# Optimization experiments

Measured on AMD Instinct MI355X. Metric: run time of the kernel, lower is better.

Reference implementation:

```python
import jax, jax.numpy as jnp
import numpy as np

B, S, D, H = 16, 784, 768, 12
DH = D // H  # 64


def rotate_half(x):
    # (x1, x2, x3, x4) -> (-x2, x1, -x4, x3), interleaved
    x_even = x[..., ::2]
    x_odd = x[..., 1::2]
    return jnp.stack((-x_odd, x_even), axis=-1).reshape(x.shape)


def setup_inputs() -> dict:
    key = jax.random.key(0)
    ks = jax.random.split(key, 12)
    s = 0.02
    return {
        "hidden_states": jax.random.normal(ks[0], (B, S, D), jnp.float32),
        "rotary_pos_emb": jax.random.uniform(ks[1], (B, S, DH), jnp.float32) * 6.28,
        "wq": jax.random.normal(ks[2], (D, D), jnp.float32) * s,
        "bq": jax.random.normal(ks[3], (D,), jnp.float32) * s,
        "wk": jax.random.normal(ks[4], (D, D), jnp.float32) * s,
        "bk": jax.random.normal(ks[5], (D,), jnp.float32) * s,
        "wv": jax.random.normal(ks[6], (D, D), jnp.float32) * s,
        "bv": jax.random.normal(ks[7], (D,), jnp.float32) * s,
        "wo": jax.random.normal(ks[8], (D, D), jnp.float32) * s,
        "bo": jax.random.normal(ks[9], (D,), jnp.float32) * s,
    }


def reference(hidden_states, rotary_pos_emb, wq, bq, wk, bk, wv, bv, wo, bo):
    scale = DH ** -0.5
    # Linear: x @ W^T + b; reshape to [B, H, S, DH]
    def proj(w, b):
        y = jnp.einsum("bsd,ed->bse", hidden_states, w) + b
        return y.reshape(B, S, H, DH).transpose(0, 2, 1, 3)

    q = proj(wq, bq)
    k = proj(wk, bk)
    v = proj(wv, bv)

    # RoPE: freqs [B, S, DH] -> [B, 1, S, DH] broadcast over heads
    cos = jnp.cos(rotary_pos_emb)[:, None, :, :]
    sin = jnp.sin(rotary_pos_emb)[:, None, :, :]
    q = q * cos + rotate_half(q) * sin
    k = k * cos + rotate_half(k) * sin

    attn = jnp.einsum("bhqd,bhkd->bhqk", q, k) * scale
    attn = jax.nn.softmax(attn, axis=-1)
    out = jnp.einsum("bhqk,bhkd->bhqd", attn, v)
    out = out.transpose(0, 2, 1, 3).reshape(B, S, D)
    out = jnp.einsum("bsd,ed->bse", out, wo) + bo
    return out
```

## Files before the change

### kernel.cpp

```cpp
#include <hip/hip_runtime.h>
#include <cstdint>
#include <cstddef>

constexpr int kB  = 16;
constexpr int kS  = 784;
constexpr int kD  = 768;
constexpr int kH  = 12;
constexpr int kM  = kB * kS;
constexpr int kSP = 832;

typedef __attribute__((ext_vector_type(8))) short bf16x8;
typedef __attribute__((ext_vector_type(4))) float floatx4;

__device__ __forceinline__ unsigned short f2bf(float x) {
    union { float f; unsigned int u; } v; v.f = x;
    unsigned int r = v.u + 0x7fffu + ((v.u >> 16) & 1u);
    return (unsigned short)(r >> 16);
}
__device__ __forceinline__ float bf2f(unsigned short h) {
    union { unsigned int u; float f; } v; v.u = ((unsigned int)h) << 16;
    return v.f;
}

__device__ __forceinline__ float fast_exp2(float x) {
#if __has_builtin(__builtin_amdgcn_exp2f)
    return __builtin_amdgcn_exp2f(x);
#else
    return __expf(x * 0.69314718055994531f);
#endif
}

__device__ __forceinline__ unsigned cvtpk(float lo, float hi) {
    unsigned r;
    asm("v_cvt_pk_bf16_f32 %0, %1, %2" : "=v"(r) : "v"(lo), "v"(hi));
    return r;
}
__device__ __forceinline__ void pl32(unsigned &a, unsigned &b) {
    asm("v_permlane32_swap_b32 %0, %1" : "+v"(a), "+v"(b));
}
__device__ __forceinline__ void pl16(unsigned &a, unsigned &b) {
    asm("v_permlane16_swap_b32 %0, %1" : "+v"(a), "+v"(b));
}
__device__ __forceinline__ bf16x8 mk8(unsigned a, unsigned b, unsigned c, unsigned d) {
    union { unsigned u[4]; bf16x8 v; } f;
    f.u[0] = a; f.u[1] = b; f.u[2] = c; f.u[3] = d; return f.v;
}

__device__ __forceinline__ void gload_lds16(const void* g, void* l) {
    __builtin_amdgcn_global_load_lds(
        (const __attribute__((address_space(1))) void*)g,
        (__attribute__((address_space(3))) void*)l,
        16, 0, 0);
}

constexpr int kHsF4   = (kM * kD) / 4;
constexpr int kWF4    = (kD * kD) / 4;
constexpr int kPreTot = kHsF4 + 4 * kWF4 + (kM * 64) / 4;

__global__ __launch_bounds__(256)
void convert_pre(const float* __restrict__ hs, const float* __restrict__ rot,
                 const float* __restrict__ wq, const float* __restrict__ wk,
                 const float* __restrict__ wv, const float* __restrict__ wo,
                 const float* __restrict__ bq, const float* __restrict__ bk,
                 const float* __restrict__ bv,
                 unsigned short* __restrict__ hsB, unsigned short* __restrict__ wB,
                 unsigned int* __restrict__ csT, float* __restrict__ biasC)
{
    const int i = blockIdx.x * 256 + threadIdx.x;
    if (i < kHsF4) {
        float4 v = ((const float4*)hs)[i];
        ushort4 o = { f2bf(v.x), f2bf(v.y), f2bf(v.z), f2bf(v.w) };
        ((ushort4*)hsB)[i] = o;
    } else if (i < kHsF4 + 4 * kWF4) {
        const int j = i - kHsF4;
        const int w = j / kWF4, jj = j - w * kWF4;
        const float* src = (w == 0) ? wq : (w == 1) ? wk : (w == 2) ? wv : wo;
        float4 v = ((const float4*)src)[jj];
        ushort4 o = { f2bf(v.x), f2bf(v.y), f2bf(v.z), f2bf(v.w) };
        ((ushort4*)(wB + (size_t)w * (kD * kD)))[jj] = o;
    } else if (i < kPreTot) {
        const int j = i - kHsF4 - 4 * kWF4;
        float4 v = ((const float4*)rot)[j];
        float a[4] = { v.x, v.y, v.z, v.w };
        #pragma unroll
        for (int e = 0; e < 4; ++e) {
            float s, c;
            __sincosf(a[e], &s, &c);
            csT[j * 4 + e] = (unsigned)f2bf(c) | ((unsigned)f2bf(s) << 16);
        }
    } else {
        const int j = i - kPreTot;
        if (j < 3 * kD)
            biasC[j] = (j < kD) ? bq[j] : (j < 2 * kD) ? bk[j - kD] : bv[j - 2 * kD];
    }
}

enum { MODE_QKV = 0, MODE_OUT = 1 };

#define BARR  __builtin_amdgcn_s_barrier()
#define LGK0  asm volatile("s_waitcnt lgkmcnt(0)" ::: "memory")
#define VM4   asm volatile("s_waitcnt vmcnt(4)" ::: "memory")
#define VM0   asm volatile("s_waitcnt vmcnt(0)" ::: "memory")
#define PRIO1 __builtin_amdgcn_s_setprio(1)
#define PRIO0 __builtin_amdgcn_s_setprio(0)

#define LDA4(KS, RB, MQ) do{ \
  afr[0]=*(const bf16x8*)(rdA##KS+(RB)+((MQ)+0)*4096); \
  afr[1]=*(const bf16x8*)(rdA##KS+(RB)+((MQ)+1)*4096); \
  afr[2]=*(const bf16x8*)(rdA##KS+(RB)+((MQ)+2)*4096); \
  afr[3]=*(const bf16x8*)(rdA##KS+(RB)+((MQ)+3)*4096); }while(0)

#define LDB4(KS, RB) do{ \
  bfr[0]=*(const bf16x8*)(rdB##KS+(RB)); \
  bfr[1]=*(const bf16x8*)(rdB##KS+(RB)+8192); \
  bfr[2]=*(const bf16x8*)(rdB##KS+(RB)+16384); \
  bfr[3]=*(const bf16x8*)(rdB##KS+(RB)+24576); }while(0)

#define MFMA16(MQ) do{ _Pragma("unroll") for(int nt=0;nt<4;++nt){ \
  acc[(MQ)  ][nt]=__builtin_amdgcn_mfma_f32_16x16x32_bf16(afr[0],bfr[nt],acc[(MQ)  ][nt],0,0,0); \
  acc[(MQ)+1][nt]=__builtin_amdgcn_mfma_f32_16x16x32_bf16(afr[1],bfr[nt],acc[(MQ)+1][nt],0,0,0); \
  acc[(MQ)+2][nt]=__builtin_amdgcn_mfma_f32_16x16x32_bf16(afr[2],bfr[nt],acc[(MQ)+2][nt],0,0,0); \
  acc[(MQ)+3][nt]=__builtin_amdgcn_mfma_f32_16x16x32_bf16(afr[3],bfr[nt],acc[(MQ)+3][nt],0,0,0); \
}}while(0)

#define KTILE(RB, SB, KT) do{ \
   LDA4(0, RB, 0); LDB4(0, RB); \
    if ((KT) <= 10) { stA(1, (KT)+1, SB); stB(1, (KT)+1, SB); } \
    BARR; LGK0; PRIO1; MFMA16(0); PRIO0; BARR; \
   LDA4(0, RB, 4); \
    BARR; LGK0; PRIO1; MFMA16(4); PRIO0; BARR; \
   LDA4(1, RB, 0); LDB4(1, RB); \
    BARR; LGK0; PRIO1; MFMA16(0); PRIO0; BARR; \
   LDA4(1, RB, 4); \
    if ((KT) <= 9) { stA(0, (KT)+2, RB); stB(0, (KT)+2, RB); VM4; } \
    else if ((KT) == 10) { VM0; } \
    BARR; LGK0; PRIO1; MFMA16(4); PRIO0; BARR; \
}while(0)

template<int MODE>
__global__ __launch_bounds__(512, 2)
void gemm8(const unsigned short* __restrict__ A, const unsigned short* __restrict__ W,
           const float* __restrict__ bias, const unsigned int* __restrict__ csT,
           unsigned short* __restrict__ Qp, unsigned short* __restrict__ Kp,
           unsigned short* __restrict__ Vtp, float* __restrict__ Op)
{
    constexpr int NTL = (MODE == MODE_QKV) ? 9 : 3;

    __shared__ unsigned short SM[65536];

    const int lin   = blockIdx.x;
    const int group = lin / (8 * NTL);
    const int rem   = lin - group * (8 * NTL);
    int m_tile, n_tile;
    if (group < 6) { m_tile = group * 8 + (rem & 7); n_tile = rem >> 3; }
    else           { m_tile = 48; n_tile = rem; }
    const int m0 = m_tile * 256;
    const int n0 = n_tile * 256;

    const int tid  = threadIdx.x;
    const int wave = tid >> 6;
    const int lane = tid & 63;
    const int quad = lane >> 4, l16 = lane & 15;
    const int wm = wave & 1;
    const int wn = wave >> 1;

    const int l8  = lane >> 3;
    const int sc  = (lane & 7) ^ l8;
    const unsigned short* gA0 = A + (size_t)(m0 + wave * 16 + l8) * kD + sc * 8;
    const unsigned short* gA1 = gA0 + (size_t)8 * kD;
    const unsigned short* gB0 = W + (size_t)(n0 + wave * 16 + l8) * kD + sc * 8;
    const unsigned short* gB1 = gB0 + (size_t)8 * kD;
    char* smc = (char*)SM;

    auto stA = [&](int h, int kt, int bufoff) {
        const int off = h * 98304 + kt * 64;
        gload_lds16(gA0 + off, smc + bufoff + h * 16384 + wave * 2048);
        gload_lds16(gA1 + off, smc + bufoff + h * 16384 + wave * 2048 + 1024);
    };
    auto stB = [&](int h, int kt, int bufoff) {
        const int off = h * 98304 + kt * 64;
        gload_lds16(gB0 + off, smc + 65536 + bufoff + h * 16384 + wave * 2048);
        gload_lds16(gB1 + off, smc + 65536 + bufoff + h * 16384 + wave * 2048 + 1024);
    };

    const int swz0 = ((quad    ) ^ (l16 & 7)) * 16;
    const int swz1 = ((quad + 4) ^ (l16 & 7)) * 16;
    const char* rdA0 = (const char*)SM + (wm * 16 + l16) * 128 + swz0;
    const char* rdA1 = (const char*)SM + (wm * 16 + l16) * 128 + swz1;
    const char* rdB0 = (const char*)SM + 65536 + (wn * 16 + l16) * 128 + swz0;
    const char* rdB1 = (const char*)SM + 65536 + (wn * 16 + l16) * 128 + swz1;

    floatx4 acc[8][4];
    #pragma unroll
    for (int m = 0; m < 8; ++m)
        #pragma unroll
        for (int nt = 0; nt < 4; ++nt)
            acc[m][nt] = {0.f, 0.f, 0.f, 0.f};
    bf16x8 afr[4], bfr[4];

    stA(0, 0, 0);      stB(0, 0, 0);
    stA(1, 0, 0);      stB(1, 0, 0);
    stA(0, 1, 32768);  stB(0, 1, 32768);
    VM4;
    BARR;

    #pragma unroll
    for (int ktp = 0; ktp < 6; ++ktp) {
        KTILE(0,     32768, ktp * 2);
        KTILE(32768, 0,     ktp * 2 + 1);
    }

    if constexpr (MODE == MODE_OUT) {
        #pragma unroll
        for (int nt = 0; nt < 4; ++nt) {
            const int n = n0 + nt * 64 + wn * 16 + l16;
            const float bv = bias[n];
            #pragma unroll
            for (int m = 0; m < 8; ++m)
                #pragma unroll
                for (int r = 0; r < 4; ++r) {
                    const int mm = m0 + m * 32 + wm * 16 + quad * 4 + r;
                    Op[(size_t)mm * kD + n] = acc[m][nt][r] + bv;
                }
        }
    } else {
        const int proj = n_tile / 3;
        if (proj < 2) {
            unsigned short* dst = proj ? Kp : Qp;
            const float scale = proj ? 1.0f : 0.125f * 1.44269504088896341f;
            #pragma unroll
            for (int nt = 0; nt < 4; ++nt) {
                const int n = n0 + nt * 64 + wn * 16 + l16;
                const float bv = bias[n];
                const int col = n - proj * kD;
                const int dh = col & 63;
                const int odd = l16 & 1;
                #pragma unroll
                for (int m = 0; m < 8; ++m)
                    #pragma unroll
                    for (int r = 0; r < 4; ++r) {
                        const int mm = m0 + m * 32 + wm * 16 + quad * 4 + r;
                        const float val = acc[m][nt][r] + bv;
                        const float px = __shfl_xor(val, 1);
                        const unsigned u = csT[(size_t)mm * 64 + dh];
                        const float c = bf2f((unsigned short)(u & 0xffffu));
                        const float s = bf2f((unsigned short)(u >> 16));
                        const float out = odd ? (val * c + px * s) : (val * c - px * s);
                        dst[(size_t)mm * kD + col] = f2bf(out * scale);
                    }
            }
        } else {
            #pragma unroll
            for (int nt = 0; nt < 4; ++nt) {
                const int n = n0 + nt * 64 + wn * 16 + l16;
                const float bv = bias[n];
                const int col = n - 2 * kD;
                const int h = col >> 6, dh = col & 63;
                #pragma unroll
                for (int m = 0; m < 8; ++m) {
                    const int m_r0 = m0 + m * 32 + wm * 16 + quad * 4;
                    const int b = m_r0 / kS;
                    const int s = m_r0 - b * kS;
                    ushort4 pk;
                    pk.x = f2bf(acc[m][nt][0] + bv);
                    pk.y = f2bf(acc[m][nt][1] + bv);
                    pk.z = f2bf(acc[m][nt][2] + bv);
                    pk.w = f2bf(acc[m][nt][3] + bv);
                    *(ushort4*)(Vtp + (size_t)((b * kH + h) * 64 + dh) * kSP + s) = pk;
                }
            }
        }
    }
}

__global__ __launch_bounds__(256)
void flash_attn(const unsigned short* __restrict__ Qg,
                const unsigned short* __restrict__ Kg,
                const unsigned short* __restrict__ Vtg,
                unsigned short* __restrict__ Og)
{
    __shared__ unsigned short KV[3][8192];

    const int lin   = blockIdx.x;
    const int group = lin / 56;
    const int rem   = lin - group * 56;
    const int bh = group * 8 + (rem & 7);
    const int qt = rem >> 3;
    const int b = bh / kH, h = bh - b * kH;
    const int tid = threadIdx.x, wave = tid >> 6, lane = tid & 63;
    const int quad = lane >> 4, l16 = lane & 15;
    const int q0 = qt * 128;
    const size_t rowBase = (size_t)(b * kS) * kD + h * 64;

    #pragma unroll
    for (int j = 0; j < 4; ++j) {
        const int idx = (wave * 4 + j) * 64 + lane;
        const int row = idx >> 3, slot = idx & 7, seg = slot ^ (row & 7);
        gload_lds16(Qg + rowBase + (size_t)(q0 + row) * kD + seg * 8,
                    &KV[0][(wave * 4 + j) * 512]);
    }
    __syncthreads();
    bf16x8 aq[2][2];
    #pragma unroll
    for (int mt = 0; mt < 2; ++mt)
        #pragma unroll
        for (int ch = 0; ch < 2; ++ch) {
            const int row = wave * 32 + mt * 16 + l16;
            const int slot = (ch * 4 + quad) ^ (row & 7);
            aq[mt][ch] = *(const bf16x8*)&KV[0][row * 64 + slot * 8];
        }
    __syncthreads();

    const int cidx0 = wave * 128 + lane;
    const int crow0 = cidx0 >> 3, cseg0 = (cidx0 & 7) ^ (crow0 & 7);
    const int cidx1 = cidx0 + 64;
    const int crow1 = cidx1 >> 3, cseg1 = (cidx1 & 7) ^ (crow1 & 7);

    auto stage = [&](int kt, int buf) {
        const int kr = kt * 64;
        gload_lds16(Kg + rowBase + (size_t)(kr + crow0) * kD + cseg0 * 8,
                    &KV[buf][wave * 1024]);
        gload_lds16(Vtg + (size_t)(bh * 64 + crow0) * kSP + kr + cseg0 * 8,
                    &KV[buf][4096 + wave * 1024]);
        gload_lds16(Kg + rowBase + (size_t)(kr + crow1) * kD + cseg1 * 8,
                    &KV[buf][wave * 1024 + 512]);
        gload_lds16(Vtg + (size_t)(bh * 64 + crow1) * kSP + kr + cseg1 * 8,
                    &KV[buf][4096 + wave * 1024 + 512]);
    };

    stage(0, 0);
    stage(1, 1);

    floatx4 oacc[2][4];
    #pragma unroll
    for (int mt = 0; mt < 2; ++mt)
        #pragma unroll
        for (int nt = 0; nt < 4; ++nt)
            oacc[mt][nt] = {0.f, 0.f, 0.f, 0.f};
    floatx4 lsum[2];
    lsum[0] = {0.f, 0.f, 0.f, 0.f};
    lsum[1] = {0.f, 0.f, 0.f, 0.f};
    const bf16x8 onesb = { 16256, 16256, 16256, 16256,
                           16256, 16256, 16256, 16256 };

    int cur = 0;
    int pre = 2;
    for (int kt = 0; kt < 13; ++kt) {
        asm volatile("s_barrier" ::: "memory");
        if (kt < 11) stage(kt + 2, pre);
        if (kt < 11)       asm volatile("s_waitcnt vmcnt(8)" ::: "memory");
        else if (kt == 11) asm volatile("s_waitcnt vmcnt(4)" ::: "memory");
        else               asm volatile("s_waitcnt vmcnt(0)" ::: "memory");
        asm volatile("s_barrier" ::: "memory");

        const unsigned short* Ks = &KV[cur][0];
        const unsigned short* Vs = &KV[cur][4096];

        bf16x8 bk[4][2];
        #pragma unroll
        for (int nt = 0; nt < 4; ++nt)
            #pragma unroll
            for (int ch = 0; ch < 2; ++ch) {
                const int row = nt * 16 + l16;
                const int slot = (ch * 4 + quad) ^ (row & 7);
                bk[nt][ch] = *(const bf16x8*)&Ks[row * 64 + slot * 8];
            }

        floatx4 sc[4][2];
        __builtin_amdgcn_s_setprio(1);
        #pragma unroll
        for (int nt = 0; nt < 4; ++nt)
            #pragma unroll
            for (int mt = 0; mt < 2; ++mt) {
                sc[nt][mt] = {0.f, 0.f, 0.f, 0.f};
                sc[nt][mt] = __builtin_amdgcn_mfma_f32_16x16x32_bf16(
                    bk[nt][0], aq[mt][0], sc[nt][mt], 0, 0, 0);
                sc[nt][mt] = __builtin_amdgcn_mfma_f32_16x16x32_bf16(
                    bk[nt][1], aq[mt][1], sc[nt][mt], 0, 0, 0);
            }
        __builtin_amdgcn_s_setprio(0);

        if (kt == 12) {
            #pragma unroll
            for (int nt = 1; nt < 4; ++nt)
                #pragma unroll
                for (int mt = 0; mt < 2; ++mt)
                    #pragma unroll
                    for (int r = 0; r < 4; ++r) sc[nt][mt][r] = -1e30f;
        }

        #pragma unroll
        for (int nt = 0; nt < 4; ++nt)
            #pragma unroll
            for (int mt = 0; mt < 2; ++mt)
                #pragma unroll
                for (int r = 0; r < 4; ++r)
                    sc[nt][mt][r] = fast_exp2(sc[nt][mt][r]);

        bf16x8 ap[2][2];
        #pragma unroll
        for (int mt = 0; mt < 2; ++mt) {
            unsigned L0 = cvtpk(sc[0][mt][0], sc[0][mt][1]);
            unsigned H0 = cvtpk(sc[0][mt][2], sc[0][mt][3]);
            unsigned L1 = cvtpk(sc[1][mt][0], sc[1][mt][1]);
            unsigned H1 = cvtpk(sc[1][mt][2], sc[1][mt][3]);
            unsigned L2 = cvtpk(sc[2][mt][0], sc[2][mt][1]);
            unsigned H2 = cvtpk(sc[2][mt][2], sc[2][mt][3]);
            unsigned L3 = cvtpk(sc[3][mt][0], sc[3][mt][1]);
            unsigned H3 = cvtpk(sc[3][mt][2], sc[3][mt][3]);
            pl32(L0, L1); pl16(L0, L1);
            pl32(H0, H1); pl16(H0, H1);
            ap[mt][0] = mk8(L0, H0, L1, H1);
            pl32(L2, L3); pl16(L2, L3);
            pl32(H2, H3); pl16(H2, H3);
            ap[mt][1] = mk8(L2, H2, L3, H3);
        }

        __builtin_amdgcn_s_setprio(1);
        #pragma unroll
        for (int ks = 0; ks < 2; ++ks) {
            #pragma unroll
            for (int nt = 0; nt < 4; ++nt) {
                const int row = nt * 16 + l16;
                const int slot = (ks * 4 + quad) ^ (row & 7);
                const bf16x8 bv = *(const bf16x8*)&Vs[row * 64 + slot * 8];
                #pragma unroll
                for (int mt = 0; mt < 2; ++mt)
                    oacc[mt][nt] = __builtin_amdgcn_mfma_f32_16x16x32_bf16(
                        ap[mt][ks], bv, oacc[mt][nt], 0, 0, 0);
            }
            #pragma unroll
            for (int mt = 0; mt < 2; ++mt)
                lsum[mt] = __builtin_amdgcn_mfma_f32_16x16x32_bf16(
                    ap[mt][ks], onesb, lsum[mt], 0, 0, 0);
        }
        __builtin_amdgcn_s_setprio(0);

        cur = (cur == 2) ? 0 : cur + 1;
        pre = (pre == 2) ? 0 : pre + 1;
    }

    #pragma unroll
    for (int mt = 0; mt < 2; ++mt)
        #pragma unroll
        for (int r = 0; r < 4; ++r) {
            const int srow = q0 + wave * 32 + mt * 16 + quad * 4 + r;
            if (srow < kS) {
                const float inv = 1.0f / lsum[mt][r];
                #pragma unroll
                for (int nt = 0; nt < 4; ++nt)
                    Og[rowBase + (size_t)srow * kD + nt * 16 + l16] =
                        f2bf(oacc[mt][nt][r] * inv);
            }
        }
}

extern "C" void kernel_launch(void* const* d_in, const int* in_sizes, int n_in,
                              void* d_out, int out_size, void* d_ws, size_t ws_size,
                              hipStream_t stream)
{
    (void)in_sizes; (void)n_in; (void)out_size; (void)ws_size;
    const float* hs  = (const float*)d_in[0];
    const float* rot = (const float*)d_in[1];
    const float* wq  = (const float*)d_in[2];
    const float* bq  = (const float*)d_in[3];
    const float* wk  = (const float*)d_in[4];
    const float* bk  = (const float*)d_in[5];
    const float* wv  = (const float*)d_in[6];
    const float* bv  = (const float*)d_in[7];
    const float* wo  = (const float*)d_in[8];
    const float* bo  = (const float*)d_in[9];

    char* ws = (char*)d_ws;
    unsigned short* hsB  = (unsigned short*)ws;
    unsigned short* wB   = (unsigned short*)(ws + 19267584);
    unsigned int*   csT  = (unsigned int*)(ws + 23986176);
    float*          biasC= (float*)(ws + 27197440);
    unsigned short* Q    = (unsigned short*)(ws + 27206656);
    unsigned short* K    = (unsigned short*)(ws + 46474240);
    unsigned short* Vt   = (unsigned short*)(ws + 65741824);
    unsigned short* O    = hsB;

    convert_pre<<<dim3(12505), dim3(256), 0, stream>>>(hs, rot, wq, wk, wv, wo, bq, bk, bv,
                                                       hsB, wB, csT, biasC);
    gemm8<MODE_QKV><<<dim3(441), dim3(512), 0, stream>>>(
        hsB, wB, biasC, csT, Q, K, Vt, nullptr);
    flash_attn<<<dim3(7 * 192), dim3(256), 0, stream>>>(Q, K, Vt, O);
    gemm8<MODE_OUT><<<dim3(147), dim3(512), 0, stream>>>(
        O, wB + 3 * kD * kD, bo, nullptr, nullptr, nullptr, nullptr, (float*)d_out);
}
```

Baseline: 246.2 us.

## Replace 256x256 8-wave GEMM with 128x128 4-wave triple-buffered GEMM

Both projection GEMMs drop the 256x256 tile (512 threads, 128 KB LDS, K-step 64, double buffer). They now use 128x128 tiles with 256 threads, K-step 32 and a triple-buffered LDS ring of 48 KB with a new swizzle. The launch bound asks for three blocks per CU. The goal is more blocks (1764/588 instead of 441/147) to fix the wave-quantization tail on 256 CUs and raise occupancy. The cost is lower arithmetic intensity per tile, more global and L2 traffic, and more barriers per unit of MFMA work.

Result: slower. 269.5 us (+9.5%).

```diff
diff --git a/kernel.cpp b/kernel.cpp
--- a/kernel.cpp
+++ b/kernel.cpp
@@ -104,58 +104,38 @@
 #define PRIO1 __builtin_amdgcn_s_setprio(1)
 #define PRIO0 __builtin_amdgcn_s_setprio(0)
 
-#define LDA4(KS, RB, MQ) do{ \
-  afr[0]=*(const bf16x8*)(rdA##KS+(RB)+((MQ)+0)*4096); \
-  afr[1]=*(const bf16x8*)(rdA##KS+(RB)+((MQ)+1)*4096); \
-  afr[2]=*(const bf16x8*)(rdA##KS+(RB)+((MQ)+2)*4096); \
-  afr[3]=*(const bf16x8*)(rdA##KS+(RB)+((MQ)+3)*4096); }while(0)
-
-#define LDB4(KS, RB) do{ \
-  bfr[0]=*(const bf16x8*)(rdB##KS+(RB)); \
-  bfr[1]=*(const bf16x8*)(rdB##KS+(RB)+8192); \
-  bfr[2]=*(const bf16x8*)(rdB##KS+(RB)+16384); \
-  bfr[3]=*(const bf16x8*)(rdB##KS+(RB)+24576); }while(0)
-
-#define MFMA16(MQ) do{ _Pragma("unroll") for(int nt=0;nt<4;++nt){ \
-  acc[(MQ)  ][nt]=__builtin_amdgcn_mfma_f32_16x16x32_bf16(afr[0],bfr[nt],acc[(MQ)  ][nt],0,0,0); \
-  acc[(MQ)+1][nt]=__builtin_amdgcn_mfma_f32_16x16x32_bf16(afr[1],bfr[nt],acc[(MQ)+1][nt],0,0,0); \
-  acc[(MQ)+2][nt]=__builtin_amdgcn_mfma_f32_16x16x32_bf16(afr[2],bfr[nt],acc[(MQ)+2][nt],0,0,0); \
-  acc[(MQ)+3][nt]=__builtin_amdgcn_mfma_f32_16x16x32_bf16(afr[3],bfr[nt],acc[(MQ)+3][nt],0,0,0); \
-}}while(0)
-
-#define KTILE(RB, SB, KT) do{ \
-   LDA4(0, RB, 0); LDB4(0, RB); \
-    if ((KT) <= 10) { stA(1, (KT)+1, SB); stB(1, (KT)+1, SB); } \
-    BARR; LGK0; PRIO1; MFMA16(0); PRIO0; BARR; \
-   LDA4(0, RB, 4); \
-    BARR; LGK0; PRIO1; MFMA16(4); PRIO0; BARR; \
-   LDA4(1, RB, 0); LDB4(1, RB); \
-    BARR; LGK0; PRIO1; MFMA16(0); PRIO0; BARR; \
-   LDA4(1, RB, 4); \
-    if ((KT) <= 9) { stA(0, (KT)+2, RB); stB(0, (KT)+2, RB); VM4; } \
-    else if ((KT) == 10) { VM0; } \
-    BARR; LGK0; PRIO1; MFMA16(4); PRIO0; BARR; \
+#define KTILE4(CUR, NX2, KT) do{ \
+    if ((KT) <= 21) stg((KT) + 2, NX2); \
+    _Pragma("unroll") for (int m = 0; m < 4; ++m) \
+        afr[m] = *(const bf16x8*)(rdA + (CUR)*16384 + m*1024); \
+    _Pragma("unroll") for (int nt = 0; nt < 4; ++nt) \
+        bfr[nt] = *(const bf16x8*)(rdB + (CUR)*16384 + nt*1024); \
+    BARR; LGK0; PRIO1; \
+    _Pragma("unroll") for (int m = 0; m < 4; ++m) \
+        _Pragma("unroll") for (int nt = 0; nt < 4; ++nt) \
+            acc[m][nt] = __builtin_amdgcn_mfma_f32_16x16x32_bf16( \
+                afr[m], bfr[nt], acc[m][nt], 0, 0, 0); \
+    PRIO0; \
+    if ((KT) <= 21) { VM4; } else if ((KT) == 22) { VM0; } \
+    BARR; \
 }while(0)
 
 template<int MODE>
-__global__ __launch_bounds__(512, 2)
-void gemm8(const unsigned short* __restrict__ A, const unsigned short* __restrict__ W,
+__global__ __launch_bounds__(256, 3)
+void gemm4(const unsigned short* __restrict__ A, const unsigned short* __restrict__ W,
            const float* __restrict__ bias, const unsigned int* __restrict__ csT,
            unsigned short* __restrict__ Qp, unsigned short* __restrict__ Kp,
            unsigned short* __restrict__ Vtp, float* __restrict__ Op)
 {
-    constexpr int NTL = (MODE == MODE_QKV) ? 9 : 3;
-
-    __shared__ unsigned short SM[65536];
-
-    const int lin   = blockIdx.x;
-    const int group = lin / (8 * NTL);
-    const int rem   = lin - group * (8 * NTL);
-    int m_tile, n_tile;
-    if (group < 6) { m_tile = group * 8 + (rem & 7); n_tile = rem >> 3; }
-    else           { m_tile = 48; n_tile = rem; }
-    const int m0 = m_tile * 256;
-    const int n0 = n_tile * 256;
+    constexpr int NTL = (MODE == MODE_QKV) ? 18 : 6;
+
+    __shared__ unsigned short SM[24576];
+
+    const int lin    = blockIdx.x;
+    const int m_tile = lin / NTL;
+    const int n_tile = lin - m_tile * NTL;
+    const int m0 = m_tile * 128;
+    const int n0 = n_tile * 128;
 
     const int tid  = threadIdx.x;
     const int wave = tid >> 6;
@@ -164,82 +144,77 @@
     const int wm = wave & 1;
     const int wn = wave >> 1;
 
-    const int l8  = lane >> 3;
-    const int sc  = (lane & 7) ^ l8;
-    const unsigned short* gA0 = A + (size_t)(m0 + wave * 16 + l8) * kD + sc * 8;
-    const unsigned short* gA1 = gA0 + (size_t)8 * kD;
-    const unsigned short* gB0 = W + (size_t)(n0 + wave * 16 + l8) * kD + sc * 8;
-    const unsigned short* gB1 = gB0 + (size_t)8 * kD;
+    const int srow = wave * 16 + (lane >> 2);
+    const int sc   = (lane & 3) ^ ((lane >> 3) & 3);
+    const unsigned short* gA0 = A + (size_t)(m0 + srow) * kD + sc * 8;
+    const unsigned short* gA1 = gA0 + (size_t)64 * kD;
+    const unsigned short* gB0 = W + (size_t)(n0 + srow) * kD + sc * 8;
+    const unsigned short* gB1 = gB0 + (size_t)64 * kD;
     char* smc = (char*)SM;
 
-    auto stA = [&](int h, int kt, int bufoff) {
-        const int off = h * 98304 + kt * 64;
-        gload_lds16(gA0 + off, smc + bufoff + h * 16384 + wave * 2048);
-        gload_lds16(gA1 + off, smc + bufoff + h * 16384 + wave * 2048 + 1024);
+    auto stg = [&](int kt, int buf) {
+        const int off = kt * 32;
+        char* base = smc + buf * 16384;
+        gload_lds16(gA0 + off, base + wave * 1024);
+        gload_lds16(gA1 + off, base + 4096  + wave * 1024);
+        gload_lds16(gB0 + off, base + 8192  + wave * 1024);
+        gload_lds16(gB1 + off, base + 12288 + wave * 1024);
     };
-    auto stB = [&](int h, int kt, int bufoff) {
-        const int off = h * 98304 + kt * 64;
-        gload_lds16(gB0 + off, smc + 65536 + bufoff + h * 16384 + wave * 2048);
-        gload_lds16(gB1 + off, smc + 65536 + bufoff + h * 16384 + wave * 2048 + 1024);
-    };
-
-    const int swz0 = ((quad    ) ^ (l16 & 7)) * 16;
-    const int swz1 = ((quad + 4) ^ (l16 & 7)) * 16;
-    const char* rdA0 = (const char*)SM + (wm * 16 + l16) * 128 + swz0;
-    const char* rdA1 = (const char*)SM + (wm * 16 + l16) * 128 + swz1;
-    const char* rdB0 = (const char*)SM + 65536 + (wn * 16 + l16) * 128 + swz0;
-    const char* rdB1 = (const char*)SM + 65536 + (wn * 16 + l16) * 128 + swz1;
-
-    floatx4 acc[8][4];
+
+    const int sw = (quad ^ ((l16 >> 1) & 3)) * 16;
+    const char* rdA = smc + (wm * 64 + l16) * 64 + sw;
+    const char* rdB = smc + 8192 + (wn * 64 + l16) * 64 + sw;
+
+    floatx4 acc[4][4];
     #pragma unroll
-    for (int m = 0; m < 8; ++m)
+    for (int m = 0; m < 4; ++m)
         #pragma unroll
         for (int nt = 0; nt < 4; ++nt)
             acc[m][nt] = {0.f, 0.f, 0.f, 0.f};
     bf16x8 afr[4], bfr[4];
 
-    stA(0, 0, 0);      stB(0, 0, 0);
-    stA(1, 0, 0);      stB(1, 0, 0);
-    stA(0, 1, 32768);  stB(0, 1, 32768);
+    stg(0, 0);
+    stg(1, 1);
     VM4;
     BARR;
 
-    #pragma unroll
-    for (int ktp = 0; ktp < 6; ++ktp) {
-        KTILE(0,     32768, ktp * 2);
-        KTILE(32768, 0,     ktp * 2 + 1);
+    for (int t8 = 0; t8 < 8; ++t8) {
+        const int kt = t8 * 3;
+        KTILE4(0, 2, kt);
+        KTILE4(1, 0, kt + 1);
+        KTILE4(2, 1, kt + 2);
     }
 
     if constexpr (MODE == MODE_OUT) {
         #pragma unroll
         for (int nt = 0; nt < 4; ++nt) {
-            const int n = n0 + nt * 64 + wn * 16 + l16;
+            const int n = n0 + wn * 64 + nt * 16 + l16;
             const float bv = bias[n];
             #pragma unroll
-            for (int m = 0; m < 8; ++m)
+            for (int m = 0; m < 4; ++m)
                 #pragma unroll
                 for (int r = 0; r < 4; ++r) {
-                    const int mm = m0 + m * 32 + wm * 16 + quad * 4 + r;
+                    const int mm = m0 + wm * 64 + m * 16 + quad * 4 + r;
                     Op[(size_t)mm * kD + n] = acc[m][nt][r] + bv;
                 }
         }
     } else {
-        const int proj = n_tile / 3;
+        const int proj = n_tile / 6;
         if (proj < 2) {
             unsigned short* dst = proj ? Kp : Qp;
             const float scale = proj ? 1.0f : 0.125f * 1.44269504088896341f;
             #pragma unroll
             for (int nt = 0; nt < 4; ++nt) {
-                const int n = n0 + nt * 64 + wn * 16 + l16;
+                const int n = n0 + wn * 64 + nt * 16 + l16;
                 const float bv = bias[n];
                 const int col = n - proj * kD;
                 const int dh = col & 63;
                 const int odd = l16 & 1;
                 #pragma unroll
-                for (int m = 0; m < 8; ++m)
+                for (int m = 0; m < 4; ++m)
                     #pragma unroll
                     for (int r = 0; r < 4; ++r) {
-                        const int mm = m0 + m * 32 + wm * 16 + quad * 4 + r;
+                        const int mm = m0 + wm * 64 + m * 16 + quad * 4 + r;
                         const float val = acc[m][nt][r] + bv;
                         const float px = __shfl_xor(val, 1);
                         const unsigned u = csT[(size_t)mm * 64 + dh];
@@ -252,13 +227,13 @@
         } else {
             #pragma unroll
             for (int nt = 0; nt < 4; ++nt) {
-                const int n = n0 + nt * 64 + wn * 16 + l16;
+                const int n = n0 + wn * 64 + nt * 16 + l16;
                 const float bv = bias[n];
                 const int col = n - 2 * kD;
                 const int h = col >> 6, dh = col & 63;
                 #pragma unroll
-                for (int m = 0; m < 8; ++m) {
-                    const int m_r0 = m0 + m * 32 + wm * 16 + quad * 4;
+                for (int m = 0; m < 4; ++m) {
+                    const int m_r0 = m0 + wm * 64 + m * 16 + quad * 4;
                     const int b = m_r0 / kS;
                     const int s = m_r0 - b * kS;
                     ushort4 pk;
@@ -483,9 +458,9 @@
 
     convert_pre<<<dim3(12505), dim3(256), 0, stream>>>(hs, rot, wq, wk, wv, wo, bq, bk, bv,
                                                        hsB, wB, csT, biasC);
-    gemm8<MODE_QKV><<<dim3(441), dim3(512), 0, stream>>>(
+    gemm4<MODE_QKV><<<dim3(1764), dim3(256), 0, stream>>>(
         hsB, wB, biasC, csT, Q, K, Vt, nullptr);
     flash_attn<<<dim3(7 * 192), dim3(256), 0, stream>>>(Q, K, Vt, O);
-    gemm8<MODE_OUT><<<dim3(147), dim3(512), 0, stream>>>(
+    gemm4<MODE_OUT><<<dim3(588), dim3(256), 0, stream>>>(
         O, wB + 3 * kD * kD, bo, nullptr, nullptr, nullptr, nullptr, (float*)d_out);
 }
```
